# Optimization experiments

Hardware: AMD Instinct MI355X
Metric: run time of the kernel (lower is better)

## Reference

```python
import jax, jax.numpy as jnp
import numpy as np

B, L, D, R = 16, 256, 1024, 128

def setup_inputs() -> dict:
    key = jax.random.key(0)
    k1, k2 = jax.random.split(key)
    batch = jax.random.normal(k1, (B, L, D), dtype=jnp.float32)
    # proj initialized uniform(-0.05, 0.05) in the original
    proj = jax.random.uniform(k2, (D, R), dtype=jnp.float32, minval=-0.05, maxval=0.05)
    return {"batch": batch, "proj": proj}

def reference(batch, proj):
    # [B, L, R] projected embeddings
    t = jnp.matmul(batch, proj)
    # all-pairs squared L2 distances: sum_r (t[b,i,r] - t[b,j,r])^2 -> [B, L, L]
    diffs = t[:, :, None, :] - t[:, None, :, :]  # [B, L, L, R]
    squared_distances = jnp.sum(diffs * diffs, axis=-1)
    return squared_distances
```

## Files before the change

kernel.cpp:

```cpp
#include <hip/hip_runtime.h>
#include <stdint.h>

#define B_ 16
#define L_ 256
#define D_ 1024
#define R_ 128
#define M_ (B_*L_)

typedef short short8 __attribute__((ext_vector_type(8)));
typedef float f32x4 __attribute__((ext_vector_type(4)));

__device__ __forceinline__ unsigned short f2bf(float f) {
  union { float f; unsigned int u; } v; v.f = f;
  unsigned int r = v.u + 0x7FFFu + ((v.u >> 16) & 1u);
  return (unsigned short)(r >> 16);
}
__device__ __forceinline__ float bf2f(unsigned short s) {
  union { unsigned int u; float f; } v; v.u = ((unsigned int)s) << 16;
  return v.f;
}
__device__ __forceinline__ void gload_lds16(const void* g, void* l) {
  __builtin_amdgcn_global_load_lds(
      (const __attribute__((address_space(1))) unsigned int*)g,
      (__attribute__((address_space(3))) unsigned int*)l, 16, 0, 0);
}

__global__ __launch_bounds__(256) void k0_transpose_cast(
    const float* __restrict__ P, unsigned short* __restrict__ PbT) {
  int id = blockIdx.x * 256 + threadIdx.x;
  int n  = id & 127;
  int kc = id >> 7;
  union { unsigned short s[8]; uint4 v; } u;
#pragma unroll
  for (int j = 0; j < 8; ++j) u.s[j] = f2bf(P[(kc * 8 + j) * R_ + n]);
  *reinterpret_cast<uint4*>(&PbT[(size_t)n * D_ + kc * 8]) = u.v;
}

__global__ __launch_bounds__(256) void k1_gemm(
    const float* __restrict__ X, const unsigned short* __restrict__ PbT,
    unsigned short* __restrict__ Tb) {
  __shared__ unsigned short sX[2][16 * 128];
  __shared__ unsigned short sP[2][64 * 128];

  const int tid  = threadIdx.x;
  const int lane = tid & 63;
  const int w    = tid >> 6;
  const int lb   = (blockIdx.x & 7) * 64 + (blockIdx.x >> 3);
  const int m0   = (lb >> 1) * 16;
  const int nb0  = (lb & 1) * 64;

  f32x4 acc;
  acc[0] = 0.f; acc[1] = 0.f; acc[2] = 0.f; acc[3] = 0.f;

  auto stage = [&](int buf, int kt) {
    const int k0 = kt * 128;
#pragma unroll
    for (int i = 0; i < 2; ++i) {
      int c = tid + 256 * i;
      int row = c >> 5;
      int kq  = (c & 31) * 4;
      float4 xv = *reinterpret_cast<const float4*>(&X[(size_t)(m0 + row) * D_ + k0 + kq]);
      uint2 p;
      p.x = (unsigned int)f2bf(xv.x) | ((unsigned int)f2bf(xv.y) << 16);
      p.y = (unsigned int)f2bf(xv.z) | ((unsigned int)f2bf(xv.w) << 16);
      int byte_in_row = (kq * 2) ^ ((row & 7) << 4);
      *reinterpret_cast<uint2*>(reinterpret_cast<char*>(&sX[buf][0]) + row * 256 + byte_in_row) = p;
    }
#pragma unroll
    for (int i = 0; i < 4; ++i) {
      int c = tid + 256 * i;
      int row = c >> 4, ch = c & 15;
      gload_lds16(&PbT[(size_t)(nb0 + row) * D_ + k0 + ((ch ^ (row & 7)) * 8)],
                  reinterpret_cast<char*>(&sP[buf][0]) + c * 16);
    }
  };

  auto compute = [&](int buf) {
    const char* xb = reinterpret_cast<const char*>(&sX[buf][0]);
    const char* pb = reinterpret_cast<const char*>(&sP[buf][0]);
#pragma unroll
    for (int s = 0; s < 4; ++s) {
      int koffb = s * 64 + ((lane >> 4) << 4);
      int ar = lane & 15;
      short8 a = *reinterpret_cast<const short8*>(xb + ar * 256 + (koffb ^ ((ar & 7) << 4)));
      int br = w * 16 + (lane & 15);
      short8 b = *reinterpret_cast<const short8*>(pb + br * 256 + (koffb ^ ((br & 7) << 4)));
      acc = __builtin_amdgcn_mfma_f32_16x16x32_bf16(a, b, acc, 0, 0, 0);
    }
  };

  stage(0, 0);
  __syncthreads();
  int buf = 0;
#pragma unroll
  for (int kt = 0; kt < 8; ++kt) {
    if (kt < 7) stage(buf ^ 1, kt + 1);
    compute(buf);
    __syncthreads();
    buf ^= 1;
  }

  const int col = lane & 15;
#pragma unroll
  for (int q = 0; q < 4; ++q) {
    int row = ((lane >> 4) << 2) + q;
    Tb[(size_t)(m0 + row) * R_ + nb0 + w * 16 + col] = f2bf(acc[q]);
  }
}

__global__ __launch_bounds__(256) void k2_gram(
    const unsigned short* __restrict__ Tb, float* __restrict__ Out) {
  __shared__ unsigned short sI[16 * 128];
  __shared__ unsigned short sJ[64 * 128];
  __shared__ float nI[16], nJ[64];

  const int tid  = threadIdx.x;
  const int lane = tid & 63;
  const int w    = tid >> 6;
  const int blk  = blockIdx.x;
  const int b    = blk >> 6;
  const int it   = (blk >> 2) & 15;
  const int jq   = blk & 3;

  {
    int row = tid >> 4, ch = tid & 15;
    gload_lds16(&Tb[(size_t)(b * L_ + it * 16 + row) * R_ + ((ch ^ (row & 7)) * 8)],
                reinterpret_cast<char*>(sI) + tid * 16);
  }
#pragma unroll
  for (int i = 0; i < 4; ++i) {
    int c = tid + 256 * i;
    int row = c >> 4, ch = c & 15;
    gload_lds16(&Tb[(size_t)(b * L_ + jq * 64 + row) * R_ + ((ch ^ (row & 7)) * 8)],
                reinterpret_cast<char*>(sJ) + c * 16);
  }
  __syncthreads();

  if (tid < 160) {
    int row = tid >> 1, h = tid & 1;
    const char* base = (row < 16) ? reinterpret_cast<const char*>(sI)
                                  : reinterpret_cast<const char*>(sJ);
    int r = (row < 16) ? row : row - 16;
    float s = 0.f;
#pragma unroll
    for (int j = 0; j < 8; ++j) {
      short8 v = *reinterpret_cast<const short8*>(base + r * 256 + ((h * 128 + j * 16) ^ ((r & 7) << 4)));
#pragma unroll
      for (int e = 0; e < 8; ++e) { float f = bf2f((unsigned short)v[e]); s += f * f; }
    }
    s += __shfl_xor(s, 1);
    if (h == 0) { if (row < 16) nI[row] = s; else nJ[row - 16] = s; }
  }

  f32x4 acc;
  acc[0] = 0.f; acc[1] = 0.f; acc[2] = 0.f; acc[3] = 0.f;
  const char* ib = reinterpret_cast<const char*>(sI);
  const char* jb = reinterpret_cast<const char*>(sJ);
#pragma unroll
  for (int s = 0; s < 4; ++s) {
    int koffb = s * 64 + ((lane >> 4) << 4);
    int ar = lane & 15;
    short8 a = *reinterpret_cast<const short8*>(ib + ar * 256 + (koffb ^ ((ar & 7) << 4)));
    int br = w * 16 + (lane & 15);
    short8 bv = *reinterpret_cast<const short8*>(jb + br * 256 + (koffb ^ ((br & 7) << 4)));
    acc = __builtin_amdgcn_mfma_f32_16x16x32_bf16(a, bv, acc, 0, 0, 0);
  }
  __syncthreads();

  const int col = lane & 15;
  const int jj = w * 16 + col;
  const float nj = nJ[jj];
#pragma unroll
  for (int q = 0; q < 4; ++q) {
    int ir = ((lane >> 4) << 2) + q;
    float v = nI[ir] + nj - 2.0f * acc[q];
    Out[(size_t)(b * L_ + it * 16 + ir) * L_ + jq * 64 + jj] = fmaxf(v, 0.0f);
  }
}

extern "C" void kernel_launch(void* const* d_in, const int* in_sizes, int n_in,
                              void* d_out, int out_size, void* d_ws, size_t ws_size,
                              hipStream_t stream) {
  const float* X = (const float*)d_in[0];
  const float* P = (const float*)d_in[1];
  float* Out = (float*)d_out;
  char* ws = (char*)d_ws;
  unsigned short* PbT = (unsigned short*)ws;
  unsigned short* Tb  = (unsigned short*)(ws + (size_t)R_ * D_ * 2);

  k0_transpose_cast<<<64, 256, 0, stream>>>(P, PbT);
  k1_gemm<<<M_ / 16 * 2, 256, 0, stream>>>(X, PbT, Tb);
  k2_gram<<<B_ * 16 * 4, 256, 0, stream>>>(Tb, Out);
}
```

Measured before the change: 22.53 us.

## Software-pipeline GEMM stage with register prefetch of X and manual waitcnt

The projection GEMM loop is restructured so that fp32 X tiles are prefetched into registers two k-steps ahead. The bf16 cast and LDS write happen after the MFMA compute of the current buffer, and the P tile's async LDS loads are issued at the same point. The two __syncthreads per iteration are replaced by one explicit s_waitcnt (vmcnt(2)) plus s_barrier, so the global latency of X overlaps with compute. This costs extra registers, and correctness now depends on hand-counted vmcnt ordering.

New measurement: 20.83 us. 1.08x faster.

```diff
diff --git a/kernel.cpp b/kernel.cpp
--- a/kernel.cpp
+++ b/kernel.cpp
@@ -52,20 +52,30 @@
   f32x4 acc;
   acc[0] = 0.f; acc[1] = 0.f; acc[2] = 0.f; acc[3] = 0.f;
 
-  auto stage = [&](int buf, int kt) {
-    const int k0 = kt * 128;
+  float4 xs[2][2];
+
+  auto loadX = [&](float4* slot, int kt) {
 #pragma unroll
     for (int i = 0; i < 2; ++i) {
       int c = tid + 256 * i;
-      int row = c >> 5;
-      int kq  = (c & 31) * 4;
-      float4 xv = *reinterpret_cast<const float4*>(&X[(size_t)(m0 + row) * D_ + k0 + kq]);
+      int row = c >> 5, kq = (c & 31) * 4;
+      slot[i] = *reinterpret_cast<const float4*>(&X[(size_t)(m0 + row) * D_ + kt * 128 + kq]);
+    }
+  };
+  auto writeX = [&](int buf, const float4* slot) {
+#pragma unroll
+    for (int i = 0; i < 2; ++i) {
+      int c = tid + 256 * i;
+      int row = c >> 5, kq = (c & 31) * 4;
       uint2 p;
-      p.x = (unsigned int)f2bf(xv.x) | ((unsigned int)f2bf(xv.y) << 16);
-      p.y = (unsigned int)f2bf(xv.z) | ((unsigned int)f2bf(xv.w) << 16);
+      p.x = (unsigned int)f2bf(slot[i].x) | ((unsigned int)f2bf(slot[i].y) << 16);
+      p.y = (unsigned int)f2bf(slot[i].z) | ((unsigned int)f2bf(slot[i].w) << 16);
       int byte_in_row = (kq * 2) ^ ((row & 7) << 4);
       *reinterpret_cast<uint2*>(reinterpret_cast<char*>(&sX[buf][0]) + row * 256 + byte_in_row) = p;
     }
+  };
+  auto issueP = [&](int buf, int kt) {
+    const int k0 = kt * 128;
 #pragma unroll
     for (int i = 0; i < 4; ++i) {
       int c = tid + 256 * i;
@@ -74,7 +84,6 @@
                   reinterpret_cast<char*>(&sP[buf][0]) + c * 16);
     }
   };
-
   auto compute = [&](int buf) {
     const char* xb = reinterpret_cast<const char*>(&sX[buf][0]);
     const char* pb = reinterpret_cast<const char*>(&sP[buf][0]);
@@ -89,15 +98,22 @@
     }
   };
 
-  stage(0, 0);
-  __syncthreads();
-  int buf = 0;
+  loadX(xs[0], 0);
+  issueP(0, 0);
+  loadX(xs[1], 1);
+  writeX(0, xs[0]);
+
 #pragma unroll
   for (int kt = 0; kt < 8; ++kt) {
-    if (kt < 7) stage(buf ^ 1, kt + 1);
+    const int buf = kt & 1;
+    if (kt == 7) asm volatile("s_waitcnt vmcnt(0) lgkmcnt(0)" ::: "memory");
+    else         asm volatile("s_waitcnt vmcnt(2) lgkmcnt(0)" ::: "memory");
+    __builtin_amdgcn_sched_barrier(0);
+    __builtin_amdgcn_s_barrier();
     compute(buf);
-    __syncthreads();
-    buf ^= 1;
+    if (kt < 7) issueP(buf ^ 1, kt + 1);
+    if (kt < 6) loadX(xs[kt & 1], kt + 2);
+    if (kt < 7) writeX(buf ^ 1, xs[(kt + 1) & 1]);
   }
 
   const int col = lane & 15;
```

## Drop LDS staging, load MFMA operands from global directly, fuse row norms into GEMM

Applied to the files above, without the earlier changes.

Both the projection GEMM and the Gram kernel now read MFMA operands straight from global memory into registers, skipping the LDS tiles and barriers. The GEMM converts fp32 to bf16 with packed cvt instructions. The GEMM epilogue also computes per-row squared norms of the rounded bf16 projections into a workspace buffer, so the Gram kernel no longer recomputes them. This removes LDS traffic and synchronisation, at the cost of redundant, less coalesced global and cache reads, since each wave reloads shared rows.

Result: slower. 39.09 us (+73.5%).

```diff
diff --git a/kernel.cpp b/kernel.cpp
--- a/kernel.cpp
+++ b/kernel.cpp
@@ -19,11 +19,6 @@
   union { unsigned int u; float f; } v; v.u = ((unsigned int)s) << 16;
   return v.f;
 }
-__device__ __forceinline__ void gload_lds16(const void* g, void* l) {
-  __builtin_amdgcn_global_load_lds(
-      (const __attribute__((address_space(1))) unsigned int*)g,
-      (__attribute__((address_space(3))) unsigned int*)l, 16, 0, 0);
-}
 
 __global__ __launch_bounds__(256) void k0_transpose_cast(
     const float* __restrict__ P, unsigned short* __restrict__ PbT) {
@@ -36,11 +31,10 @@
   *reinterpret_cast<uint4*>(&PbT[(size_t)n * D_ + kc * 8]) = u.v;
 }
 
-__global__ __launch_bounds__(256) void k1_gemm(
+__global__ __launch_bounds__(256, 4) void k1_gemm(
     const float* __restrict__ X, const unsigned short* __restrict__ PbT,
-    unsigned short* __restrict__ Tb) {
-  __shared__ unsigned short sX[2][16 * 128];
-  __shared__ unsigned short sP[2][64 * 128];
+    unsigned short* __restrict__ Tb, float* __restrict__ Nrm2) {
+  __shared__ float nacc[16][4];
 
   const int tid  = threadIdx.x;
   const int lane = tid & 63;
@@ -49,71 +43,54 @@
   const int m0   = (lb >> 1) * 16;
   const int nb0  = (lb & 1) * 64;
 
+  const int ar = lane & 15;
+  const int ko = (lane >> 4) * 8;
+
+  const float*          xrow = X   + (size_t)(m0 + ar) * D_;
+  const unsigned short* prow = PbT + (size_t)(nb0 + w * 16 + ar) * D_;
+
   f32x4 acc;
   acc[0] = 0.f; acc[1] = 0.f; acc[2] = 0.f; acc[3] = 0.f;
 
-  auto stage = [&](int buf, int kt) {
-    const int k0 = kt * 128;
-#pragma unroll
-    for (int i = 0; i < 2; ++i) {
-      int c = tid + 256 * i;
-      int row = c >> 5;
-      int kq  = (c & 31) * 4;
-      float4 xv = *reinterpret_cast<const float4*>(&X[(size_t)(m0 + row) * D_ + k0 + kq]);
-      uint2 p;
-      p.x = (unsigned int)f2bf(xv.x) | ((unsigned int)f2bf(xv.y) << 16);
-      p.y = (unsigned int)f2bf(xv.z) | ((unsigned int)f2bf(xv.w) << 16);
-      int byte_in_row = (kq * 2) ^ ((row & 7) << 4);
-      *reinterpret_cast<uint2*>(reinterpret_cast<char*>(&sX[buf][0]) + row * 256 + byte_in_row) = p;
-    }
-#pragma unroll
-    for (int i = 0; i < 4; ++i) {
-      int c = tid + 256 * i;
-      int row = c >> 4, ch = c & 15;
-      gload_lds16(&PbT[(size_t)(nb0 + row) * D_ + k0 + ((ch ^ (row & 7)) * 8)],
-                  reinterpret_cast<char*>(&sP[buf][0]) + c * 16);
-    }
-  };
-
-  auto compute = [&](int buf) {
-    const char* xb = reinterpret_cast<const char*>(&sX[buf][0]);
-    const char* pb = reinterpret_cast<const char*>(&sP[buf][0]);
+#pragma unroll 2
+  for (int kt = 0; kt < 8; ++kt) {
 #pragma unroll
     for (int s = 0; s < 4; ++s) {
-      int koffb = s * 64 + ((lane >> 4) << 4);
-      int ar = lane & 15;
-      short8 a = *reinterpret_cast<const short8*>(xb + ar * 256 + (koffb ^ ((ar & 7) << 4)));
-      int br = w * 16 + (lane & 15);
-      short8 b = *reinterpret_cast<const short8*>(pb + br * 256 + (koffb ^ ((br & 7) << 4)));
-      acc = __builtin_amdgcn_mfma_f32_16x16x32_bf16(a, b, acc, 0, 0, 0);
+      const int k = kt * 128 + s * 32 + ko;
+      float4 xa = *reinterpret_cast<const float4*>(xrow + k);
+      float4 xb = *reinterpret_cast<const float4*>(xrow + k + 4);
+      union { unsigned int u[4]; short8 s8; } cvt;
+      asm("v_cvt_pk_bf16_f32 %0, %1, %2" : "=v"(cvt.u[0]) : "v"(xa.x), "v"(xa.y));
+      asm("v_cvt_pk_bf16_f32 %0, %1, %2" : "=v"(cvt.u[1]) : "v"(xa.z), "v"(xa.w));
+      asm("v_cvt_pk_bf16_f32 %0, %1, %2" : "=v"(cvt.u[2]) : "v"(xb.x), "v"(xb.y));
+      asm("v_cvt_pk_bf16_f32 %0, %1, %2" : "=v"(cvt.u[3]) : "v"(xb.z), "v"(xb.w));
+      short8 b = *reinterpret_cast<const short8*>(prow + k);
+      acc = __builtin_amdgcn_mfma_f32_16x16x32_bf16(cvt.s8, b, acc, 0, 0, 0);
     }
-  };
-
-  stage(0, 0);
-  __syncthreads();
-  int buf = 0;
-#pragma unroll
-  for (int kt = 0; kt < 8; ++kt) {
-    if (kt < 7) stage(buf ^ 1, kt + 1);
-    compute(buf);
-    __syncthreads();
-    buf ^= 1;
   }
 
   const int col = lane & 15;
 #pragma unroll
   for (int q = 0; q < 4; ++q) {
-    int row = ((lane >> 4) << 2) + q;
-    Tb[(size_t)(m0 + row) * R_ + nb0 + w * 16 + col] = f2bf(acc[q]);
+    const int row = ((lane >> 4) << 2) + q;
+    unsigned short hv = f2bf(acc[q]);
+    Tb[(size_t)(m0 + row) * R_ + nb0 + w * 16 + col] = hv;
+    float tr = bf2f(hv);
+    float s = tr * tr;
+    s += __shfl_xor(s, 1); s += __shfl_xor(s, 2);
+    s += __shfl_xor(s, 4); s += __shfl_xor(s, 8);
+    if (col == 0) nacc[row][w] = s;
+  }
+  __syncthreads();
+  if (tid < 16) {
+    float t = nacc[tid][0] + nacc[tid][1] + nacc[tid][2] + nacc[tid][3];
+    Nrm2[(size_t)(lb & 1) * M_ + m0 + tid] = t;
   }
 }
 
-__global__ __launch_bounds__(256) void k2_gram(
-    const unsigned short* __restrict__ Tb, float* __restrict__ Out) {
-  __shared__ unsigned short sI[16 * 128];
-  __shared__ unsigned short sJ[64 * 128];
-  __shared__ float nI[16], nJ[64];
-
+__global__ __launch_bounds__(256, 4) void k2_gram(
+    const unsigned short* __restrict__ Tb, const float* __restrict__ Nrm2,
+    float* __restrict__ Out) {
   const int tid  = threadIdx.x;
   const int lane = tid & 63;
   const int w    = tid >> 6;
@@ -122,59 +99,30 @@
   const int it   = (blk >> 2) & 15;
   const int jq   = blk & 3;
 
-  {
-    int row = tid >> 4, ch = tid & 15;
-    gload_lds16(&Tb[(size_t)(b * L_ + it * 16 + row) * R_ + ((ch ^ (row & 7)) * 8)],
-                reinterpret_cast<char*>(sI) + tid * 16);
-  }
-#pragma unroll
-  for (int i = 0; i < 4; ++i) {
-    int c = tid + 256 * i;
-    int row = c >> 4, ch = c & 15;
-    gload_lds16(&Tb[(size_t)(b * L_ + jq * 64 + row) * R_ + ((ch ^ (row & 7)) * 8)],
-                reinterpret_cast<char*>(sJ) + c * 16);
-  }
-  __syncthreads();
+  const int ar = lane & 15;
+  const int ko = (lane >> 4) * 8;
 
-  if (tid < 160) {
-    int row = tid >> 1, h = tid & 1;
-    const char* base = (row < 16) ? reinterpret_cast<const char*>(sI)
-                                  : reinterpret_cast<const char*>(sJ);
-    int r = (row < 16) ? row : row - 16;
-    float s = 0.f;
-#pragma unroll
-    for (int j = 0; j < 8; ++j) {
-      short8 v = *reinterpret_cast<const short8*>(base + r * 256 + ((h * 128 + j * 16) ^ ((r & 7) << 4)));
-#pragma unroll
-      for (int e = 0; e < 8; ++e) { float f = bf2f((unsigned short)v[e]); s += f * f; }
-    }
-    s += __shfl_xor(s, 1);
-    if (h == 0) { if (row < 16) nI[row] = s; else nJ[row - 16] = s; }
-  }
+  const unsigned short* irow = Tb + (size_t)(b * L_ + it * 16 + ar) * R_;
+  const unsigned short* jrow = Tb + (size_t)(b * L_ + jq * 64 + w * 16 + ar) * R_;
 
   f32x4 acc;
   acc[0] = 0.f; acc[1] = 0.f; acc[2] = 0.f; acc[3] = 0.f;
-  const char* ib = reinterpret_cast<const char*>(sI);
-  const char* jb = reinterpret_cast<const char*>(sJ);
 #pragma unroll
   for (int s = 0; s < 4; ++s) {
-    int koffb = s * 64 + ((lane >> 4) << 4);
-    int ar = lane & 15;
-    short8 a = *reinterpret_cast<const short8*>(ib + ar * 256 + (koffb ^ ((ar & 7) << 4)));
-    int br = w * 16 + (lane & 15);
-    short8 bv = *reinterpret_cast<const short8*>(jb + br * 256 + (koffb ^ ((br & 7) << 4)));
+    short8 a  = *reinterpret_cast<const short8*>(irow + s * 32 + ko);
+    short8 bv = *reinterpret_cast<const short8*>(jrow + s * 32 + ko);
     acc = __builtin_amdgcn_mfma_f32_16x16x32_bf16(a, bv, acc, 0, 0, 0);
   }
-  __syncthreads();
 
   const int col = lane & 15;
-  const int jj = w * 16 + col;
-  const float nj = nJ[jj];
+  const int jj  = jq * 64 + w * 16 + col;
+  const float nj = Nrm2[b * L_ + jj] + Nrm2[M_ + b * L_ + jj];
 #pragma unroll
   for (int q = 0; q < 4; ++q) {
-    int ir = ((lane >> 4) << 2) + q;
-    float v = nI[ir] + nj - 2.0f * acc[q];
-    Out[(size_t)(b * L_ + it * 16 + ir) * L_ + jq * 64 + jj] = fmaxf(v, 0.0f);
+    const int ir = it * 16 + ((lane >> 4) << 2) + q;
+    const float ni = Nrm2[b * L_ + ir] + Nrm2[M_ + b * L_ + ir];
+    float v = ni + nj - 2.0f * acc[q];
+    Out[(size_t)(b * L_ + ir) * L_ + jj] = fmaxf(v, 0.0f);
   }
 }
 
@@ -187,8 +135,9 @@
   char* ws = (char*)d_ws;
   unsigned short* PbT = (unsigned short*)ws;
   unsigned short* Tb  = (unsigned short*)(ws + (size_t)R_ * D_ * 2);
+  float* Nrm2 = (float*)(ws + (size_t)R_ * D_ * 2 + (size_t)M_ * R_ * 2);
 
   k0_transpose_cast<<<64, 256, 0, stream>>>(P, PbT);
-  k1_gemm<<<M_ / 16 * 2, 256, 0, stream>>>(X, PbT, Tb);
-  k2_gram<<<B_ * 16 * 4, 256, 0, stream>>>(Tb, Out);
+  k1_gemm<<<512, 256, 0, stream>>>(X, PbT, Tb, Nrm2);
+  k2_gram<<<1024, 256, 0, stream>>>(Tb, Nrm2, Out);
 }
```
